# Optimization experiments

Measured on AMD Instinct MI355X. Metric: run time of the kernel, lower is better.

The kernel has to match this reference:

```python
import jax, jax.numpy as jnp
import numpy as np


def setup_inputs() -> dict:
    key = jax.random.key(0)
    k1, k2 = jax.random.split(key)
    N, C, H, W = 8, 256, 64, 64
    K = 3
    x = jax.random.normal(k1, (N, C, H, W), dtype=jnp.float32)
    kernel = jax.random.normal(k2, (N, 1, K * K, H, W), dtype=jnp.float32)
    return {"x": x, "kernel": kernel, "kernel_size": K, "dilation": 1}


def _patches(x, K, dilation):
    # torch nn.Unfold ordering: patch index = kh*K + kw, channel slowest.
    N, C, H, W = x.shape
    pad = K // 2 * dilation
    xp = jnp.pad(x, ((0, 0), (0, 0), (pad, pad), (pad, pad)))
    # [N, C, K*K, H, W]
    return jnp.stack(
        [xp[:, :, i * dilation:i * dilation + H, j * dilation:j * dilation + W]
         for i in range(K) for j in range(K)],
        axis=2,
    )


def reference(x, kernel, kernel_size, dilation):
    patches = _patches(x, kernel_size, dilation)      # [N, C, K*K, H, W]
    return (patches * kernel).sum(axis=2)             # [N, C, H, W]
```

## Files before the change

### kernel.cpp

```cpp
#include <hip/hip_runtime.h>

constexpr int Nn = 8, Cc = 256, Hh = 64, Ww = 64;
constexpr int CHUNK = 64;

__global__ __launch_bounds__(256) void ddf_kernel(const float* __restrict__ x,
                                                  const float* __restrict__ ker,
                                                  float* __restrict__ out) {
    const int b  = blockIdx.x;
    const int cb = b & 3;
    const int h  = (b >> 2) & 63;
    const int n  = b >> 8;

    const int t  = threadIdx.x;
    const int wg = t & 15;
    const int cl = t >> 4;
    const int w0 = wg << 2;

    float4 kf[9];
    const float* kbase = ker + ((size_t)(n * 9) * Hh + h) * Ww + w0;
#pragma unroll
    for (int tap = 0; tap < 9; ++tap)
        kf[tap] = *reinterpret_cast<const float4*>(kbase + (size_t)tap * Hh * Ww);

#pragma unroll
    for (int it = 0; it < CHUNK / 16; ++it) {
        const int c = cb * CHUNK + it * 16 + cl;
        const float* xc = x + ((size_t)(n * Cc + c) * Hh) * Ww;

        float4 acc = {0.f, 0.f, 0.f, 0.f};
#pragma unroll
        for (int r = 0; r < 3; ++r) {
            const int hh = h + r - 1;
            if (hh < 0 || hh >= Hh) continue;
            const float* row = xc + (size_t)hh * Ww;

            const float4 v = *reinterpret_cast<const float4*>(row + w0);
            const float lm = (w0 > 0)       ? row[w0 - 1] : 0.f;
            const float rp = (w0 + 4 < Ww)  ? row[w0 + 4] : 0.f;

            const float4 k0 = kf[r * 3 + 0];
            const float4 k1 = kf[r * 3 + 1];
            const float4 k2 = kf[r * 3 + 2];

            acc.x += k0.x * lm  + k1.x * v.x + k2.x * v.y;
            acc.y += k0.y * v.x + k1.y * v.y + k2.y * v.z;
            acc.z += k0.z * v.y + k1.z * v.z + k2.z * v.w;
            acc.w += k0.w * v.z + k1.w * v.w + k2.w * rp;
        }
        *reinterpret_cast<float4*>(out + ((size_t)(n * Cc + c) * Hh + h) * Ww + w0) = acc;
    }
}

extern "C" void kernel_launch(void* const* d_in, const int* in_sizes, int n_in,
                              void* d_out, int out_size, void* d_ws, size_t ws_size,
                              hipStream_t stream) {
    const float* x   = (const float*)d_in[0];
    const float* ker = (const float*)d_in[1];
    float* out = (float*)d_out;

    const int grid = Nn * Hh * (Cc / CHUNK);
    ddf_kernel<<<grid, 256, 0, stream>>>(x, ker, out);
}
```

Measured before the change: 100.2 us.

## Reuse input rows across a sliding vertical window and use lane shuffles for halos

Each block now processes four consecutive output rows for its channels and keeps a rolling three-row register window, so every input row is loaded once instead of three times. The left and right halo values are taken from neighbouring lanes with wavefront shuffles rather than extra scalar global loads. The grid shrinks to 512 blocks, which reduces parallelism and raises register pressure while cutting redundant memory traffic.

```diff
diff --git a/kernel.cpp b/kernel.cpp
--- a/kernel.cpp
+++ b/kernel.cpp
@@ -1,53 +1,89 @@
 #include <hip/hip_runtime.h>
 
-constexpr int Nn = 8, Cc = 256, Hh = 64, Ww = 64;
-constexpr int CHUNK = 64;
+constexpr int Cc = 256, Hh = 64, Ww = 64;
+constexpr int NCH  = 4;
+constexpr int HSEG = 4;
+
+struct Row { float4 v; float lm, rp; };
+
+__device__ __forceinline__ Row load_row(const float* __restrict__ rowptr, bool valid,
+                                        int w0, int wstrip, int lane) {
+    Row r;
+    if (valid) r.v = *reinterpret_cast<const float4*>(rowptr + w0);
+    else       r.v = make_float4(0.f, 0.f, 0.f, 0.f);
+    const float l  = __shfl(r.v.w, (lane + 63) & 63);
+    const float rr = __shfl(r.v.x, (lane + 1) & 63);
+    r.lm = (wstrip == 0)  ? 0.f : l;
+    r.rp = (wstrip == 15) ? 0.f : rr;
+    return r;
+}
+
+__device__ __forceinline__ void conv_row(float4& acc, const Row& r,
+                                         const float4& k0, const float4& k1, const float4& k2) {
+    acc.x += k0.x * r.lm  + k1.x * r.v.x + k2.x * r.v.y;
+    acc.y += k0.y * r.v.x + k1.y * r.v.y + k2.y * r.v.z;
+    acc.z += k0.z * r.v.y + k1.z * r.v.z + k2.z * r.v.w;
+    acc.w += k0.w * r.v.z + k1.w * r.v.w + k2.w * r.rp;
+}
 
 __global__ __launch_bounds__(256) void ddf_kernel(const float* __restrict__ x,
                                                   const float* __restrict__ ker,
                                                   float* __restrict__ out) {
     const int b  = blockIdx.x;
-    const int cb = b & 3;
-    const int h  = (b >> 2) & 63;
-    const int n  = b >> 8;
+    const int hs = b & (Hh / HSEG - 1);
+    const int cb = (b >> 4) & 3;
+    const int n  = b >> 6;
+    const int h0 = hs * HSEG;
 
-    const int t  = threadIdx.x;
-    const int wg = t & 15;
-    const int cl = t >> 4;
-    const int w0 = wg << 2;
+    const int t      = threadIdx.x;
+    const int lane   = t & 63;
+    const int wstrip = t & 15;
+    const int w0     = wstrip << 2;
+    const int chl    = t >> 4;
 
-    float4 kf[9];
-    const float* kbase = ker + ((size_t)(n * 9) * Hh + h) * Ww + w0;
+    const float* kcol = ker + ((size_t)n * 9 * Hh) * Ww + w0;
+
+    const float* xc[NCH];
+    float*       oc[NCH];
 #pragma unroll
-    for (int tap = 0; tap < 9; ++tap)
-        kf[tap] = *reinterpret_cast<const float4*>(kbase + (size_t)tap * Hh * Ww);
+    for (int i = 0; i < NCH; ++i) {
+        const int c = cb * 64 + i * 16 + chl;
+        xc[i] = x   + ((size_t)(n * Cc + c) * Hh) * Ww;
+        oc[i] = out + ((size_t)(n * Cc + c) * Hh) * Ww;
+    }
+
+    Row r0[NCH], r1[NCH];
+#pragma unroll
+    for (int i = 0; i < NCH; ++i) {
+        r0[i] = load_row(xc[i] + (size_t)(h0 - 1) * Ww, h0 > 0, w0, wstrip, lane);
+        r1[i] = load_row(xc[i] + (size_t)h0 * Ww,       true,   w0, wstrip, lane);
+    }
 
 #pragma unroll
-    for (int it = 0; it < CHUNK / 16; ++it) {
-        const int c = cb * CHUNK + it * 16 + cl;
-        const float* xc = x + ((size_t)(n * Cc + c) * Hh) * Ww;
+    for (int dh = 0; dh < HSEG; ++dh) {
+        const int h = h0 + dh;
 
-        float4 acc = {0.f, 0.f, 0.f, 0.f};
+        float4 kf[9];
 #pragma unroll
-        for (int r = 0; r < 3; ++r) {
-            const int hh = h + r - 1;
-            if (hh < 0 || hh >= Hh) continue;
-            const float* row = xc + (size_t)hh * Ww;
+        for (int tap = 0; tap < 9; ++tap)
+            kf[tap] = *reinterpret_cast<const float4*>(kcol + ((size_t)tap * Hh + h) * Ww);
 
-            const float4 v = *reinterpret_cast<const float4*>(row + w0);
-            const float lm = (w0 > 0)       ? row[w0 - 1] : 0.f;
-            const float rp = (w0 + 4 < Ww)  ? row[w0 + 4] : 0.f;
+        const bool vnext = (h + 1) < Hh;
+        Row r2[NCH];
+#pragma unroll
+        for (int i = 0; i < NCH; ++i)
+            r2[i] = load_row(xc[i] + (size_t)(h + 1) * Ww, vnext, w0, wstrip, lane);
 
-            const float4 k0 = kf[r * 3 + 0];
-            const float4 k1 = kf[r * 3 + 1];
-            const float4 k2 = kf[r * 3 + 2];
-
-            acc.x += k0.x * lm  + k1.x * v.x + k2.x * v.y;
-            acc.y += k0.y * v.x + k1.y * v.y + k2.y * v.z;
-            acc.z += k0.z * v.y + k1.z * v.z + k2.z * v.w;
-            acc.w += k0.w * v.z + k1.w * v.w + k2.w * rp;
+#pragma unroll
+        for (int i = 0; i < NCH; ++i) {
+            float4 acc = make_float4(0.f, 0.f, 0.f, 0.f);
+            conv_row(acc, r0[i], kf[0], kf[1], kf[2]);
+            conv_row(acc, r1[i], kf[3], kf[4], kf[5]);
+            conv_row(acc, r2[i], kf[6], kf[7], kf[8]);
+            *reinterpret_cast<float4*>(oc[i] + (size_t)h * Ww + w0) = acc;
+            r0[i] = r1[i];
+            r1[i] = r2[i];
         }
-        *reinterpret_cast<float4*>(out + ((size_t)(n * Cc + c) * Hh + h) * Ww + w0) = acc;
     }
 }
 
@@ -58,6 +94,6 @@
     const float* ker = (const float*)d_in[1];
     float* out = (float*)d_out;
 
-    const int grid = Nn * Hh * (Cc / CHUNK);
+    const int grid = 8 * (Cc / 64) * (Hh / HSEG);
     ddf_kernel<<<grid, 256, 0, stream>>>(x, ker, out);
 }
```

Measured after the change: 96.27 us. 1.04x faster.
